# Performance work log

Measured on AMD Instinct MI355X. Metric: run time of the kernel, lower is better.

The kernel has to match this reference:

```python
import jax, jax.numpy as jnp
from jax import lax
import numpy as np

B, C, H, W = 2, 64, 128, 128
DN = ('NCHW', 'OIHW', 'NCHW')


def setup_inputs() -> dict:
    key = jax.random.key(0)
    ks = jax.random.split(key, 20)
    rn = lambda k, s, sc=0.05: jax.random.normal(k, s, dtype=jnp.float32) * sc
    inp = {
        'x': jax.random.normal(ks[0], (B, C, H, W), dtype=jnp.float32),
        'off1_w': rn(ks[1], (C, 1, 1, 15)), 'off1_b': rn(ks[2], (C,)),
        'bn1_s': 1.0 + rn(ks[3], (C,)), 'bn1_b': rn(ks[4], (C,)),
        'off2_w': rn(ks[5], (C, 1, 15, 1)), 'off2_b': rn(ks[6], (C,)),
        'bn2_s': 1.0 + rn(ks[7], (C,)), 'bn2_b': rn(ks[8], (C,)),
        'off3_w': rn(ks[9], (C, 1, 3, 3)), 'off3_b': rn(ks[10], (C,)),
        'bn3_s': 1.0 + rn(ks[11], (C,)), 'bn3_b': rn(ks[12], (C,)),
        'bal_w': rn(ks[13], (18, C, 1, 1)), 'bal_b': rn(ks[14], (18,)),
        'bn4_s': 1.0 + rn(ks[15], (18,)), 'bn4_b': rn(ks[16], (18,)),
        'dw2': rn(ks[17], (C, 1, 3, 3), 0.1),
        'dw3': rn(jax.random.fold_in(key, 101), (C, 1, 3, 3), 0.1),
        'dw4': rn(jax.random.fold_in(key, 102), (C, 1, 3, 3), 0.1),
        'dw5': rn(jax.random.fold_in(key, 103), (C, 1, 3, 3), 0.1),
        'fin_w': rn(ks[18], (C, C, 1, 1)), 'fin_b': rn(ks[19], (C,)),
        'bn5_s': 1.0 + rn(jax.random.fold_in(key, 104), (C,)),
        'bn5_b': rn(jax.random.fold_in(key, 105), (C,)),
    }
    return inp


def _dwconv(x, w, pad):
    return lax.conv_general_dilated(x, w, (1, 1), [(pad[0], pad[0]), (pad[1], pad[1])],
                                    dimension_numbers=DN, feature_group_count=x.shape[1])


def _conv1x1(x, w):
    return lax.conv_general_dilated(x, w, (1, 1), 'VALID', dimension_numbers=DN)


def _bias(x, b):
    return x + b[None, :, None, None]


def _bn(x, s, b):  # inference-form BatchNorm folded into per-channel affine
    return x * s[None, :, None, None] + b[None, :, None, None]


def _bilinear(x, py, px):
    # x: [B,C,H,W]; py/px: [B,9,H,W] float sampling coords -> [B,C,9,H,W]
    Bn, Cn, Hn, Wn = x.shape
    y0 = jnp.floor(py)
    x0 = jnp.floor(px)
    wy1 = py - y0  # fractional parts
    wx1 = px - x0
    xf = x.reshape(Bn, Cn, Hn * Wn)

    def gather(yi, xi):
        valid = (yi >= 0) & (yi <= Hn - 1) & (xi >= 0) & (xi <= Wn - 1)
        yc = jnp.clip(yi, 0, Hn - 1).astype(jnp.int32)
        xc = jnp.clip(xi, 0, Wn - 1).astype(jnp.int32)
        idx = (yc * Wn + xc).reshape(Bn, -1)  # [B, 9*H*W]
        v = jax.vmap(lambda f, i: f[:, i])(xf, idx)  # [B,C,9*H*W]
        v = v.reshape(Bn, Cn, 9, Hn, Wn)
        return v * valid[:, None].astype(x.dtype)  # zero padding outside

    g00 = gather(y0, x0)
    g01 = gather(y0, x0 + 1)
    g10 = gather(y0 + 1, x0)
    g11 = gather(y0 + 1, x0 + 1)
    wy1e = wy1[:, None]
    wx1e = wx1[:, None]
    return (g00 * (1 - wy1e) * (1 - wx1e) + g01 * (1 - wy1e) * wx1e
            + g10 * wy1e * (1 - wx1e) + g11 * wy1e * wx1e)


def _deform_dw(x, offsets, w, d):
    # depthwise DeformConv2d: kernel 3x3, stride 1, padding=d, dilation=d, groups=C
    Bn, Cn, Hn, Wn = x.shape
    off = offsets.reshape(Bn, 9, 2, Hn, Wn)  # pairs (dy, dx) per kernel tap, row-major
    ky = (jnp.arange(9) // 3 - 1).astype(x.dtype)  # [-1,-1,-1,0,0,0,1,1,1]
    kx = (jnp.arange(9) % 3 - 1).astype(x.dtype)
    hs = jnp.arange(Hn, dtype=x.dtype)
    ws = jnp.arange(Wn, dtype=x.dtype)
    # output loc h maps to input h - pad + ki*dil = h + (ki-1)*d since pad == dil == d
    py = off[:, :, 0] + (hs[:, None] + d * ky[:, None, None])[None]  # [B,9,H,W]
    px = off[:, :, 1] + (ws[None, :] + d * kx[:, None, None])[None]
    s = _bilinear(x, py, px)  # [B,C,9,H,W]
    return jnp.einsum('bckhw,ck->bchw', s, w.reshape(Cn, 9))


def reference(x, off1_w, off1_b, bn1_s, bn1_b, off2_w, off2_b, bn2_s, bn2_b,
              off3_w, off3_b, bn3_s, bn3_b, bal_w, bal_b, bn4_s, bn4_b,
              dw2, dw3, dw4, dw5, fin_w, fin_b, bn5_s, bn5_b):
    # DirectionOffsets: three depthwise convs + BN, summed, then 1x1 -> 18ch + BN
    o1 = _bn(_bias(_dwconv(x, off1_w, (0, 7)), off1_b), bn1_s, bn1_b)
    o2 = _bn(_bias(_dwconv(x, off2_w, (7, 0)), off2_b), bn2_s, bn2_b)
    o3 = _bn(_bias(_dwconv(x, off3_w, (1, 1)), off3_b), bn3_s, bn3_b)
    off = _bn(_bias(_conv1x1(o1 + o2 + o3, bal_w), bal_b), bn4_s, bn4_b)  # [B,18,H,W]
    # four deformable depthwise convs sharing the offset field
    out = (_deform_dw(x, off, dw2, 2) + _deform_dw(x, off, dw3, 3)
           + _deform_dw(x, off, dw4, 4) + _deform_dw(x, off, dw5, 5))
    out = _bn(_bias(_conv1x1(out, fin_w), fin_b), bn5_s, bn5_b) * x
    return out
```

## Files before the change

kernel.cpp:

```cpp
#include <hip/hip_runtime.h>

#define BB 2
#define CC 64
#define HH 128
#define WW 128
#define HWN (HH*WW)
#define CHW (CC*HWN)

#define BAND_H 8
#define HALO   8
#define NBAND  (HH / BAND_H)
#define LROWS  (BAND_H + 2 * HALO)
#define CPB    2
#define XPAD   8
#define XSTR   (WW + 2 * XPAD)

#define OB_H 16
#define OB_HALO 7
#define OB_ROWS (OB_H + 2 * OB_HALO)
#define OSTR 144

__global__ __launch_bounds__(256) void osum_kernel(const float* __restrict__ x,
    const float* __restrict__ w1, const float* __restrict__ b1, const float* __restrict__ s1, const float* __restrict__ g1,
    const float* __restrict__ w2, const float* __restrict__ b2, const float* __restrict__ s2, const float* __restrict__ g2,
    const float* __restrict__ w3, const float* __restrict__ b3, const float* __restrict__ s3, const float* __restrict__ g3,
    float* __restrict__ osum)
{
    __shared__ float xs[OB_ROWS * OSTR];
    int bid  = blockIdx.x;
    int band = bid & 7;
    int bc   = bid >> 3;
    int c    = bc & (CC - 1);
    int bs   = band * OB_H;
    int r_lo_v = bs - OB_HALO;

    for (int i = threadIdx.x; i < (OB_ROWS * OSTR) / 4; i += 256)
        ((float4*)xs)[i] = make_float4(0.f, 0.f, 0.f, 0.f);
    __syncthreads();

    int gstart = r_lo_v < 0 ? 0 : r_lo_v;
    int gend   = r_lo_v + OB_ROWS; if (gend > HH) gend = HH;
    int nitems = (gend - gstart) * (WW / 4);
    const float* xp = x + (size_t)bc * HWN;
    for (int i = threadIdx.x; i < nitems; i += 256) {
        int r = i >> 5, col4 = i & 31;
        int g = gstart + r;
        int lr = g - r_lo_v;
        ((float4*)xs)[lr * (OSTR / 4) + 2 + col4] = ((const float4*)(xp + g * WW))[col4];
    }
    __syncthreads();

    float W1[15], W2[15], W3[9];
    #pragma unroll
    for (int k = 0; k < 15; ++k) { W1[k] = w1[c * 15 + k]; W2[k] = w2[c * 15 + k]; }
    #pragma unroll
    for (int k = 0; k < 9; ++k) W3[k] = w3[c * 9 + k];
    float bb1 = b1[c], ss1 = s1[c], gg1 = g1[c];
    float bb2 = b2[c], ss2 = s2[c], gg2 = g2[c];
    float bb3 = b3[c], ss3 = s3[c], gg3 = g3[c];

    #pragma unroll
    for (int i = 0; i < (OB_H * WW) / 256; ++i) {
        int p = bs * WW + i * 256 + threadIdx.x;
        int h = p >> 7;
        int w = p & (WW - 1);
        int lr = h - r_lo_v;
        int base = lr * OSTR + XPAD + w;

        float a1 = 0.f;
        #pragma unroll
        for (int k = 0; k < 15; ++k) a1 += xs[base + k - 7] * W1[k];
        float a2 = 0.f;
        #pragma unroll
        for (int k = 0; k < 15; ++k) a2 += xs[base + (k - 7) * OSTR] * W2[k];
        float a3 = 0.f;
        #pragma unroll
        for (int kh = 0; kh < 3; ++kh)
            #pragma unroll
            for (int kw = 0; kw < 3; ++kw)
                a3 += xs[base + (kh - 1) * OSTR + (kw - 1)] * W3[kh * 3 + kw];

        osum[(size_t)bc * HWN + p] = (a1 + bb1) * ss1 + gg1
                                   + (a2 + bb2) * ss2 + gg2
                                   + (a3 + bb3) * ss3 + gg3;
    }
}

__global__ __launch_bounds__(256) void off_kernel(const float* __restrict__ osum,
    const float* __restrict__ balw, const float* __restrict__ balb,
    const float* __restrict__ s4, const float* __restrict__ g4,
    float* __restrict__ off)
{
    __shared__ float ls[CC * 128];
    int bid = blockIdx.x;
    int b   = bid >> 7;
    int hw0 = (bid & 127) * 128;

    const float* src = osum + (size_t)b * CHW + hw0;
    #pragma unroll
    for (int i = 0; i < 8; ++i) {
        int idx = threadIdx.x + i * 256;
        int row = idx >> 5, col4 = idx & 31;
        ((float4*)ls)[row * 32 + col4] = *(const float4*)(src + (size_t)row * HWN + col4 * 4);
    }
    __syncthreads();

    int hw = (threadIdx.x & 63) + ((threadIdx.x >> 6) & 1) * 64;
    int og = __builtin_amdgcn_readfirstlane((int)(threadIdx.x >> 7));

    float acc[9];
    #pragma unroll
    for (int j = 0; j < 9; ++j) acc[j] = 0.f;
    for (int ic = 0; ic < CC; ++ic) {
        float v = ls[ic * 128 + hw];
        #pragma unroll
        for (int j = 0; j < 9; ++j)
            acc[j] += v * balw[(og * 9 + j) * CC + ic];
    }
    #pragma unroll
    for (int j = 0; j < 9; ++j) {
        int oc = og * 9 + j;
        off[(size_t)b * (18 * HWN) + (size_t)oc * HWN + hw0 + hw] =
            (acc[j] + balb[oc]) * s4[oc] + g4[oc];
    }
}

__device__ __forceinline__ float gz(const float* __restrict__ xp, int y, int x) {
    return ((unsigned)y < (unsigned)HH && (unsigned)x < (unsigned)WW) ? xp[y * WW + x] : 0.f;
}

__global__ __launch_bounds__(256) void deform_kernel(
    const float* __restrict__ x,
    const float* __restrict__ off,
    const float* __restrict__ dw2, const float* __restrict__ dw3,
    const float* __restrict__ dw4, const float* __restrict__ dw5,
    float* __restrict__ pre)
{
    __shared__ float xs[LROWS * XSTR * CPB];

    int bid  = blockIdx.x;
    int band = bid & (NBAND - 1);
    int bcp  = bid >> 4;
    int cp   = bcp & 31;
    int b    = bcp >> 5;
    int c0   = cp * CPB;
    int bc0  = b * CC + c0;

    int r_lo_v = band * BAND_H - HALO;

    for (int i = threadIdx.x; i < (LROWS * XSTR * CPB) / 4; i += 256)
        ((float4*)xs)[i] = make_float4(0.f, 0.f, 0.f, 0.f);
    __syncthreads();

    int gstart = r_lo_v < 0 ? 0 : r_lo_v;
    int gend   = r_lo_v + LROWS; if (gend > HH) gend = HH;
    int nitems = (gend - gstart) * (WW / 4);
    const float* xp0 = x + (size_t)bc0 * HWN;
    const float* xp1 = xp0 + HWN;
    for (int i = threadIdx.x; i < nitems; i += 256) {
        int r = i >> 5, col4 = i & 31;
        int g = gstart + r;
        int lr = g - r_lo_v;
        float4 q0 = ((const float4*)(xp0 + g * WW))[col4];
        float4 q1 = ((const float4*)(xp1 + g * WW))[col4];
        ((float4*)xs)[lr * (XSTR / 2) + XPAD / 2 + col4 * 2]     = make_float4(q0.x, q1.x, q0.y, q1.y);
        ((float4*)xs)[lr * (XSTR / 2) + XPAD / 2 + col4 * 2 + 1] = make_float4(q0.z, q1.z, q0.w, q1.w);
    }
    __syncthreads();

    const float2* XS2 = (const float2*)xs;
    const float* offb = off + (size_t)b * (18 * HWN);

    #pragma unroll 1
    for (int chunk = 0; chunk < (BAND_H * WW) / 256; ++chunk) {
        int p = band * (BAND_H * WW) + chunk * 256 + (int)threadIdx.x;
        float hf = (float)(p >> 7);
        float wf = (float)(p & (WW - 1));

        float oy[9], ox[9];
        #pragma unroll
        for (int k = 0; k < 9; ++k) {
            oy[k] = offb[((size_t)(2 * k) << 14) + p];
            ox[k] = offb[((size_t)(2 * k + 1) << 14) + p];
        }

        float acc0 = 0.f, acc1 = 0.f;
        #pragma unroll
        for (int k = 0; k < 9; ++k) {
            const int ky = k / 3 - 1, kx = k % 3 - 1;
            float pyb = oy[k] + hf;
            float pxb = ox[k] + wf;
            float y0f = floorf(pyb), x0f = floorf(pxb);
            float wy = pyb - y0f, wx = pxb - x0f;
            int y0g = (int)y0f, x0g = (int)x0f;
            int y0b = y0g - r_lo_v;
            int x0b = x0g + XPAD;
            float cxa = 1.f - wx, cxb = wx;

            const int dkyLo = (ky < 0) ? -5 : (ky > 0 ? 2 : 0);
            const int dkyHi = (ky < 0) ? -2 : (ky > 0 ? 5 : 0);
            const int dkxLo = (kx < 0) ? -5 : (kx > 0 ? 2 : 0);
            const int dkxHi = (kx < 0) ? -2 : (kx > 0 ? 5 : 0);
            bool ok = (y0b + dkyLo >= 0) & (y0b + dkyHi <= LROWS - 2)
                    & (x0b + dkxLo >= 0) & (x0b + dkxHi <= XSTR - 2);

            if (ok) {
                #pragma unroll
                for (int di = 0; di < 4; ++di) {
                    const int d = di + 2;
                    int f0 = (y0b + d * ky) * XSTR + (x0b + d * kx);
                    float2 a  = XS2[f0],        bq = XS2[f0 + 1];
                    float2 cq = XS2[f0 + XSTR], dq = XS2[f0 + XSTR + 1];
                    float ra0 = cxa * a.x + cxb * bq.x;
                    float rb0 = cxa * cq.x + cxb * dq.x;
                    float ra1 = cxa * a.y + cxb * bq.y;
                    float rb1 = cxa * cq.y + cxb * dq.y;
                    float s0 = ra0 + wy * (rb0 - ra0);
                    float s1 = ra1 + wy * (rb1 - ra1);
                    const float* dwp = (di == 0) ? dw2 : (di == 1) ? dw3 : (di == 2) ? dw4 : dw5;
                    acc0 += s0 * dwp[c0 * 9 + k];
                    acc1 += s1 * dwp[(c0 + 1) * 9 + k];
                }
            } else {
                #pragma unroll
                for (int di = 0; di < 4; ++di) {
                    const int d = di + 2;
                    int yy = y0g + d * ky, xx = x0g + d * kx;
                    float v00 = gz(xp0, yy, xx),     v01 = gz(xp0, yy, xx + 1);
                    float v10 = gz(xp0, yy + 1, xx), v11 = gz(xp0, yy + 1, xx + 1);
                    float u00 = gz(xp1, yy, xx),     u01 = gz(xp1, yy, xx + 1);
                    float u10 = gz(xp1, yy + 1, xx), u11 = gz(xp1, yy + 1, xx + 1);
                    float s0 = (1.f - wy) * (cxa * v00 + cxb * v01) + wy * (cxa * v10 + cxb * v11);
                    float s1 = (1.f - wy) * (cxa * u00 + cxb * u01) + wy * (cxa * u10 + cxb * u11);
                    const float* dwp = (di == 0) ? dw2 : (di == 1) ? dw3 : (di == 2) ? dw4 : dw5;
                    acc0 += s0 * dwp[c0 * 9 + k];
                    acc1 += s1 * dwp[(c0 + 1) * 9 + k];
                }
            }
        }
        pre[((size_t)bc0 << 14) + p]       = acc0;
        pre[((size_t)(bc0 + 1) << 14) + p] = acc1;
    }
}

__global__ __launch_bounds__(256) void final_kernel(const float* __restrict__ pre,
    const float* __restrict__ finw, const float* __restrict__ finb,
    const float* __restrict__ s5, const float* __restrict__ g5,
    const float* __restrict__ x, float* __restrict__ out)
{
    __shared__ float ls[CC * 64];
    int bid = blockIdx.x;
    int b   = bid >> 8;
    int hw0 = (bid & 255) * 64;

    const float* src = pre + (size_t)b * CHW + hw0;
    #pragma unroll
    for (int i = 0; i < 4; ++i) {
        int idx = threadIdx.x + i * 256;
        int row = idx >> 4, col4 = idx & 15;
        ((float4*)ls)[row * 16 + col4] = *(const float4*)(src + (size_t)row * HWN + col4 * 4);
    }
    __syncthreads();

    int hw = threadIdx.x & 63;
    int og = __builtin_amdgcn_readfirstlane((int)(threadIdx.x >> 6));

    float acc[16];
    #pragma unroll
    for (int j = 0; j < 16; ++j) acc[j] = 0.f;
    for (int ic = 0; ic < CC; ++ic) {
        float v = ls[ic * 64 + hw];
        #pragma unroll
        for (int j = 0; j < 16; ++j)
            acc[j] += v * finw[(og * 16 + j) * CC + ic];
    }
    #pragma unroll
    for (int j = 0; j < 16; ++j) {
        int oc = og * 16 + j;
        size_t oidx = ((size_t)(b * CC + oc) << 14) + hw0 + hw;
        out[oidx] = ((acc[j] + finb[oc]) * s5[oc] + g5[oc]) * x[oidx];
    }
}

extern "C" void kernel_launch(void* const* d_in, const int* in_sizes, int n_in,
                              void* d_out, int out_size, void* d_ws, size_t ws_size,
                              hipStream_t stream) {
    const float* x      = (const float*)d_in[0];
    const float* off1_w = (const float*)d_in[1];
    const float* off1_b = (const float*)d_in[2];
    const float* bn1_s  = (const float*)d_in[3];
    const float* bn1_b  = (const float*)d_in[4];
    const float* off2_w = (const float*)d_in[5];
    const float* off2_b = (const float*)d_in[6];
    const float* bn2_s  = (const float*)d_in[7];
    const float* bn2_b  = (const float*)d_in[8];
    const float* off3_w = (const float*)d_in[9];
    const float* off3_b = (const float*)d_in[10];
    const float* bn3_s  = (const float*)d_in[11];
    const float* bn3_b  = (const float*)d_in[12];
    const float* bal_w  = (const float*)d_in[13];
    const float* bal_b  = (const float*)d_in[14];
    const float* bn4_s  = (const float*)d_in[15];
    const float* bn4_b  = (const float*)d_in[16];
    const float* dw2    = (const float*)d_in[17];
    const float* dw3    = (const float*)d_in[18];
    const float* dw4    = (const float*)d_in[19];
    const float* dw5    = (const float*)d_in[20];
    const float* fin_w  = (const float*)d_in[21];
    const float* fin_b  = (const float*)d_in[22];
    const float* bn5_s  = (const float*)d_in[23];
    const float* bn5_b  = (const float*)d_in[24];

    float* ws   = (float*)d_ws;
    float* osum = ws;
    float* off  = ws + (size_t)BB * CHW;
    float* pre  = off + (size_t)BB * 18 * HWN;

    float* out = (float*)d_out;

    osum_kernel<<<BB * CC * (HH / OB_H), 256, 0, stream>>>(x,
        off1_w, off1_b, bn1_s, bn1_b,
        off2_w, off2_b, bn2_s, bn2_b,
        off3_w, off3_b, bn3_s, bn3_b, osum);
    off_kernel<<<BB * (HWN / 128), 256, 0, stream>>>(osum, bal_w, bal_b, bn4_s, bn4_b, off);
    deform_kernel<<<BB * (CC / CPB) * NBAND, 256, 0, stream>>>(x, off, dw2, dw3, dw4, dw5, pre);
    final_kernel<<<BB * (HWN / 64), 256, 0, stream>>>(pre, fin_w, fin_b, bn5_s, bn5_b, x, out);
}
```

Baseline: 162.0 us.

## Register-block osum convs, split off_kernel finer, halve deform band height

The osum kernel now has each thread compute eight adjacent outputs from float4 shared-memory loads held in registers, so neighbouring taps are reused instead of reloaded per pixel, and it writes the results as float4 stores. The off kernel processes 64 pixels per block and splits the 18 output channels across four wave groups, which doubles the block count for better occupancy. The deform kernel's band height drops from 8 to 4, doubling its blocks at the cost of more halo reloading per output row. Register pressure in osum rises, and the halo overhead in deform grows.

```diff
diff --git a/kernel.cpp b/kernel.cpp
--- a/kernel.cpp
+++ b/kernel.cpp
@@ -7,7 +7,7 @@
 #define HWN (HH*WW)
 #define CHW (CC*HWN)
 
-#define BAND_H 8
+#define BAND_H 4
 #define HALO   8
 #define NBAND  (HH / BAND_H)
 #define LROWS  (BAND_H + 2 * HALO)
@@ -59,31 +59,62 @@
     float bb2 = b2[c], ss2 = s2[c], gg2 = g2[c];
     float bb3 = b3[c], ss3 = s3[c], gg3 = g3[c];
 
-    #pragma unroll
-    for (int i = 0; i < (OB_H * WW) / 256; ++i) {
-        int p = bs * WW + i * 256 + threadIdx.x;
-        int h = p >> 7;
-        int w = p & (WW - 1);
-        int lr = h - r_lo_v;
-        int base = lr * OSTR + XPAD + w;
-
-        float a1 = 0.f;
-        #pragma unroll
-        for (int k = 0; k < 15; ++k) a1 += xs[base + k - 7] * W1[k];
-        float a2 = 0.f;
-        #pragma unroll
-        for (int k = 0; k < 15; ++k) a2 += xs[base + (k - 7) * OSTR] * W2[k];
-        float a3 = 0.f;
-        #pragma unroll
-        for (int kh = 0; kh < 3; ++kh)
+    const float4* XS4 = (const float4*)xs;
+    int oct = threadIdx.x & 15;
+    int row = threadIdx.x >> 4;
+    int w0  = oct * 8;
+    int lr  = row + OB_HALO;
+    int h   = bs + row;
+
+    float hb[24];
+    #pragma unroll
+    for (int t = 0; t < 6; ++t) {
+        float4 q = XS4[lr * (OSTR / 4) + 2 * oct + t];
+        hb[4*t] = q.x; hb[4*t+1] = q.y; hb[4*t+2] = q.z; hb[4*t+3] = q.w;
+    }
+    float a1[8];
+    #pragma unroll
+    for (int j = 0; j < 8; ++j) {
+        float s = 0.f;
+        #pragma unroll
+        for (int k = 0; k < 15; ++k) s += hb[j + 1 + k] * W1[k];
+        a1[j] = s;
+    }
+
+    float a2[8] = {0.f,0.f,0.f,0.f,0.f,0.f,0.f,0.f};
+    #pragma unroll
+    for (int k = 0; k < 15; ++k) {
+        float4 qa = XS4[(lr + k - 7) * (OSTR / 4) + 2 + 2 * oct];
+        float4 qb = XS4[(lr + k - 7) * (OSTR / 4) + 3 + 2 * oct];
+        a2[0] += qa.x * W2[k]; a2[1] += qa.y * W2[k]; a2[2] += qa.z * W2[k]; a2[3] += qa.w * W2[k];
+        a2[4] += qb.x * W2[k]; a2[5] += qb.y * W2[k]; a2[6] += qb.z * W2[k]; a2[7] += qb.w * W2[k];
+    }
+
+    float a3[8] = {0.f,0.f,0.f,0.f,0.f,0.f,0.f,0.f};
+    #pragma unroll
+    for (int kh = 0; kh < 3; ++kh) {
+        float m[16];
+        #pragma unroll
+        for (int t = 0; t < 4; ++t) {
+            float4 q = XS4[(lr + kh - 1) * (OSTR / 4) + 1 + 2 * oct + t];
+            m[4*t] = q.x; m[4*t+1] = q.y; m[4*t+2] = q.z; m[4*t+3] = q.w;
+        }
+        #pragma unroll
+        for (int j = 0; j < 8; ++j)
             #pragma unroll
             for (int kw = 0; kw < 3; ++kw)
-                a3 += xs[base + (kh - 1) * OSTR + (kw - 1)] * W3[kh * 3 + kw];
-
-        osum[(size_t)bc * HWN + p] = (a1 + bb1) * ss1 + gg1
-                                   + (a2 + bb2) * ss2 + gg2
-                                   + (a3 + bb3) * ss3 + gg3;
-    }
+                a3[j] += m[j + kw + 3] * W3[kh * 3 + kw];
+    }
+
+    float o[8];
+    #pragma unroll
+    for (int j = 0; j < 8; ++j)
+        o[j] = (a1[j] + bb1) * ss1 + gg1
+             + (a2[j] + bb2) * ss2 + gg2
+             + (a3[j] + bb3) * ss3 + gg3;
+    float* dst = osum + (size_t)bc * HWN + h * WW + w0;
+    ((float4*)dst)[0] = make_float4(o[0], o[1], o[2], o[3]);
+    ((float4*)dst)[1] = make_float4(o[4], o[5], o[6], o[7]);
 }
 
 __global__ __launch_bounds__(256) void off_kernel(const float* __restrict__ osum,
@@ -91,38 +122,39 @@
     const float* __restrict__ s4, const float* __restrict__ g4,
     float* __restrict__ off)
 {
-    __shared__ float ls[CC * 128];
+    __shared__ float ls[CC * 64];
     int bid = blockIdx.x;
-    int b   = bid >> 7;
-    int hw0 = (bid & 127) * 128;
+    int b   = bid >> 8;
+    int hw0 = (bid & 255) * 64;
 
     const float* src = osum + (size_t)b * CHW + hw0;
     #pragma unroll
-    for (int i = 0; i < 8; ++i) {
+    for (int i = 0; i < 4; ++i) {
         int idx = threadIdx.x + i * 256;
-        int row = idx >> 5, col4 = idx & 31;
-        ((float4*)ls)[row * 32 + col4] = *(const float4*)(src + (size_t)row * HWN + col4 * 4);
-    }
-    __syncthreads();
-
-    int hw = (threadIdx.x & 63) + ((threadIdx.x >> 6) & 1) * 64;
-    int og = __builtin_amdgcn_readfirstlane((int)(threadIdx.x >> 7));
-
-    float acc[9];
-    #pragma unroll
-    for (int j = 0; j < 9; ++j) acc[j] = 0.f;
+        int row = idx >> 4, col4 = idx & 15;
+        ((float4*)ls)[row * 16 + col4] = *(const float4*)(src + (size_t)row * HWN + col4 * 4);
+    }
+    __syncthreads();
+
+    int px = threadIdx.x & 63;
+    int og = __builtin_amdgcn_readfirstlane((int)(threadIdx.x >> 6));
+    int start = (og < 2) ? og * 5 : 10 + (og - 2) * 4;
+    int cnt   = (og < 2) ? 5 : 4;
+
+    float acc[5] = {0.f, 0.f, 0.f, 0.f, 0.f};
     for (int ic = 0; ic < CC; ++ic) {
-        float v = ls[ic * 128 + hw];
-        #pragma unroll
-        for (int j = 0; j < 9; ++j)
-            acc[j] += v * balw[(og * 9 + j) * CC + ic];
-    }
-    #pragma unroll
-    for (int j = 0; j < 9; ++j) {
-        int oc = og * 9 + j;
-        off[(size_t)b * (18 * HWN) + (size_t)oc * HWN + hw0 + hw] =
-            (acc[j] + balb[oc]) * s4[oc] + g4[oc];
-    }
+        float v = ls[ic * 64 + px];
+        #pragma unroll
+        for (int j = 0; j < 5; ++j)
+            if (j < cnt) acc[j] += v * balw[(start + j) * CC + ic];
+    }
+    #pragma unroll
+    for (int j = 0; j < 5; ++j)
+        if (j < cnt) {
+            int oc = start + j;
+            off[(size_t)b * (18 * HWN) + (size_t)oc * HWN + hw0 + px] =
+                (acc[j] + balb[oc]) * s4[oc] + g4[oc];
+        }
 }
 
 __device__ __forceinline__ float gz(const float* __restrict__ xp, int y, int x) {
@@ -140,7 +172,7 @@
 
     int bid  = blockIdx.x;
     int band = bid & (NBAND - 1);
-    int bcp  = bid >> 4;
+    int bcp  = bid >> 5;
     int cp   = bcp & 31;
     int b    = bcp >> 5;
     int c0   = cp * CPB;
@@ -322,7 +354,7 @@
         off1_w, off1_b, bn1_s, bn1_b,
         off2_w, off2_b, bn2_s, bn2_b,
         off3_w, off3_b, bn3_s, bn3_b, osum);
-    off_kernel<<<BB * (HWN / 128), 256, 0, stream>>>(osum, bal_w, bal_b, bn4_s, bn4_b, off);
+    off_kernel<<<BB * (HWN / 64), 256, 0, stream>>>(osum, bal_w, bal_b, bn4_s, bn4_b, off);
     deform_kernel<<<BB * (CC / CPB) * NBAND, 256, 0, stream>>>(x, off, dw2, dw3, dw4, dw5, pre);
     final_kernel<<<BB * (HWN / 64), 256, 0, stream>>>(pre, fin_w, fin_b, bn5_s, bn5_b, x, out);
 }
```

New measurement: 168.2 us. +3.9%, slower.
